# Performance work log

Measured on AMD Instinct MI355X. Metric: run time of the kernel, lower is better.

Reference implementation:

```python
import jax, jax.numpy as jnp
import numpy as np

KERNEL_MUL = 2.0
KERNEL_NUM = 5


def _gaussian_kernel(source, target, kernel_mul=KERNEL_MUL, kernel_num=KERNEL_NUM):
    # total: [(n+m), d]
    total = jnp.concatenate([source, target], axis=0)
    n_total = total.shape[0]
    # Pairwise squared L2 via GEMM trick (same math as (total0-total1)^2.sum(-1)).
    sq = jnp.sum(total * total, axis=1)  # [(n+m)]
    l2 = sq[:, None] + sq[None, :] - 2.0 * (total @ total.T)
    l2 = jnp.maximum(l2, 0.0)  # numerical floor; exact value is >= 0
    # Bandwidth from mean off-diagonal distance; .data in torch => stop_gradient.
    denom = n_total * n_total - n_total
    bandwidth = jax.lax.stop_gradient(jnp.sum(l2)) / denom
    bandwidth = bandwidth / (kernel_mul ** (kernel_num // 2))
    # Multi-bandwidth Gaussian kernel sum (fused accumulation).
    kernels = jnp.zeros_like(l2)
    for i in range(kernel_num):
        kernels = kernels + jnp.exp(-l2 / (bandwidth * (kernel_mul ** i)))
    return kernels


def setup_inputs() -> dict:
    key = jax.random.key(0)
    k1, k2 = jax.random.split(key)
    source = jax.random.normal(k1, (4096, 512), dtype=jnp.float32)
    target = jax.random.normal(k2, (4096, 512), dtype=jnp.float32)
    return {"source": source, "target": target}


def reference(source, target):
    batch_size = source.shape[0]
    kernels = _gaussian_kernel(source, target)
    xx = jnp.mean(kernels[:batch_size, :batch_size])
    yy = jnp.mean(kernels[batch_size:, batch_size:])
    xy = jnp.mean(kernels[:batch_size, batch_size:])
    yx = jnp.mean(kernels[batch_size:, :batch_size])
    return xx + yy - xy - yx
```

## Files before the change

kernel.cpp:

```cpp
#include <hip/hip_runtime.h>

#define N_TOT 8192
#define DIMS  512

typedef __attribute__((ext_vector_type(4))) int   i32x4;
typedef __attribute__((ext_vector_type(4))) float f32x4;

__global__ __launch_bounds__(256) void prep_kernel(
    const float* __restrict__ src, const float* __restrict__ tgt,
    char* __restrict__ Tb, float* __restrict__ sq,
    float* __restrict__ colsum4, float* __restrict__ sumsqtot)
{
    __shared__ float cp[4 * 512];
    __shared__ float wss[4];
    int lane = threadIdx.x & 63;
    int wave = threadIdx.x >> 6;
    int b = blockIdx.x;

    float colacc[8];
#pragma unroll
    for (int j = 0; j < 8; j++) colacc[j] = 0.f;
    float wsum = 0.f;

#pragma unroll 4
    for (int rr = 0; rr < 8; rr++) {
        int row = b * 32 + wave * 8 + rr;
        const float* p = (row < 4096) ? (src + (size_t)row * DIMS)
                                      : (tgt + (size_t)(row - 4096) * DIMS);
        float4 v0 = *(const float4*)(p + lane * 8);
        float4 v1 = *(const float4*)(p + lane * 8 + 4);
        float vs[8] = {v0.x, v0.y, v0.z, v0.w, v1.x, v1.y, v1.z, v1.w};
        float rs = 0.f;
        int q[8];
#pragma unroll
        for (int j = 0; j < 8; j++) {
            rs += vs[j] * vs[j];
            colacc[j] += vs[j];
            q[j] = max(-127, min(127, __float2int_rn(vs[j] * 25.4f)));
        }
        unsigned lo = (q[0] & 0xff) | ((q[1] & 0xff) << 8) | ((q[2] & 0xff) << 16) | ((q[3] & 0xff) << 24);
        unsigned hi = (q[4] & 0xff) | ((q[5] & 0xff) << 8) | ((q[6] & 0xff) << 16) | ((q[7] & 0xff) << 24);
        *(uint2*)(Tb + (size_t)row * DIMS + lane * 8) = make_uint2(lo, hi);
#pragma unroll
        for (int off = 32; off; off >>= 1) rs += __shfl_down(rs, off, 64);
        if (lane == 0) { sq[row] = rs; wsum += rs; }
    }
    if (lane == 0) wss[wave] = wsum;
#pragma unroll
    for (int j = 0; j < 8; j++) cp[wave * 512 + lane * 8 + j] = colacc[j];
    __syncthreads();
    int t = threadIdx.x;
    float c0 = cp[t] + cp[512 + t] + cp[1024 + t] + cp[1536 + t];
    float c1 = cp[t + 256] + cp[512 + t + 256] + cp[1024 + t + 256] + cp[1536 + t + 256];
    int rep = (b & 3) * 512;
    atomicAdd(&colsum4[rep + t], c0);
    atomicAdd(&colsum4[rep + t + 256], c1);
    if (t == 0) atomicAdd(sumsqtot, wss[0] + wss[1] + wss[2] + wss[3]);
}

__global__ __launch_bounds__(256, 4) void mmd_main(
    const char* __restrict__ Tb, const float* __restrict__ sq,
    const float* __restrict__ colsum4, const float* __restrict__ sumsqtot,
    double* __restrict__ partial)
{
    int bb = blockIdx.x;
    int x = bb & 7;
    int c = bb >> 3;
    int lo = 4 * x;
    int hi = 60 - 4 * x;
    int I, J;
    int R1 = 8 * (4 * x + 1);
    if (c < R1) {
        J = 63 - (c >> 3);
        int r = c & 7;
        I = (r < 4) ? (lo + r) : (hi + (r - 4));
    } else {
        int c2 = c - R1;
        if (c2 < 18) {
            int r;
            if (c2 < 7)       { J = hi + 2; r = c2; }
            else if (c2 < 13) { J = hi + 1; r = c2 - 7; }
            else              { J = hi;     r = c2 - 13; }
            I = (r < 4) ? (lo + r) : (hi + (r - 4));
        } else {
            int c3 = c2 - 18;
            int S3 = 4 * (57 - 8 * x);
            if (c3 < S3) {
                J = (hi - 1) - (c3 >> 2);
                I = lo + (c3 & 3);
            } else {
                int c4 = c3 - S3;
                if (c4 < 3)      { J = lo + 2; I = lo + c4; }
                else if (c4 < 5) { J = lo + 1; I = lo + (c4 - 3); }
                else             { J = lo;     I = lo; }
            }
        }
    }

    __shared__ __align__(16) char As[128 * 128];
    __shared__ __align__(16) char Bs[128 * 128];

    int t = threadIdx.x;
    int lane = t & 63, wave = t >> 6;
    int wr = (wave >> 1) * 64, wc = (wave & 1) * 64;
    int m = lane & 15, quad = lane >> 4;

    const char* Arow = Tb + (size_t)I * 128 * DIMS;
    const char* Brow = Tb + (size_t)J * 128 * DIMS;
    int lgrp = lane >> 3;
    int gsw  = ((lane & 7) ^ lgrp) * 16;

    i32x4 acc[4][4] = {};

    for (int k0 = 0; k0 < 512; k0 += 128) {
#pragma unroll
        for (int p = 0; p < 4; p++) {
            int r = p * 32 + wave * 8 + lgrp;
            const char* ga = Arow + (size_t)r * DIMS + k0 + gsw;
            const char* gb = Brow + (size_t)r * DIMS + k0 + gsw;
            __builtin_amdgcn_global_load_lds(
                (const __attribute__((address_space(1))) void*)ga,
                (__attribute__((address_space(3))) void*)&As[(p * 32 + wave * 8) * 128], 16, 0, 0);
            __builtin_amdgcn_global_load_lds(
                (const __attribute__((address_space(1))) void*)gb,
                (__attribute__((address_space(3))) void*)&Bs[(p * 32 + wave * 8) * 128], 16, 0, 0);
        }
        __syncthreads();
#pragma unroll
        for (int ks = 0; ks < 2; ks++) {
            i32x4 af[4], bfr[4];
#pragma unroll
            for (int mi = 0; mi < 4; mi++) {
                int ra = wr + mi * 16 + m;
                af[mi] = *(const i32x4*)&As[ra * 128 + ((ks * 4 + quad) ^ (m & 7)) * 16];
            }
#pragma unroll
            for (int ni = 0; ni < 4; ni++) {
                int rb = wc + ni * 16 + m;
                bfr[ni] = *(const i32x4*)&Bs[rb * 128 + ((ks * 4 + quad) ^ (m & 7)) * 16];
            }
#pragma unroll
            for (int mi = 0; mi < 4; mi++)
#pragma unroll
                for (int ni = 0; ni < 4; ni++)
                    acc[mi][ni] = __builtin_amdgcn_mfma_i32_16x16x64_i8(
                        af[mi], bfr[ni], acc[mi][ni], 0, 0, 0);
        }
        __syncthreads();
    }
    double* shd = (double*)As;
    float*  shw = (float*)(As + 64);

    float sqa[16], sqb[4];
#pragma unroll
    for (int mi = 0; mi < 4; mi++)
#pragma unroll
        for (int r = 0; r < 4; r++)
            sqa[mi * 4 + r] = sq[I * 128 + wr + mi * 16 + quad * 4 + r];
#pragma unroll
    for (int ni = 0; ni < 4; ni++) sqb[ni] = sq[J * 128 + wc + ni * 16 + m];

    {
        float cs0 = colsum4[t] + colsum4[512 + t] + colsum4[1024 + t] + colsum4[1536 + t];
        int uu = t + 256;
        float cs1 = colsum4[uu] + colsum4[512 + uu] + colsum4[1024 + uu] + colsum4[1536 + uu];
        double c2 = (double)cs0 * (double)cs0 + (double)cs1 * (double)cs1;
#pragma unroll
        for (int off = 32; off; off >>= 1) c2 += __shfl_down(c2, off, 64);
        if (lane == 0) shd[wave] = c2;
        __syncthreads();
        if (t == 0) {
            double C2 = shd[0] + shd[1] + shd[2] + shd[3];
            double SS = (double)sumsqtot[0];
            double suml2 = 2.0 * 8192.0 * SS - 2.0 * C2;
            double denom = 8192.0 * 8192.0 - 8192.0;
            shd[4] = suml2 / denom / 4.0;
        }
        __syncthreads();
    }
    double bws = shd[4];

    float nc = (float)(-1.4426950408889634 / (16.0 * bws));
    float m2nc = -2.0f * nc * (float)(25.0 / 16129.0);
    float pa[16], pb[4];
#pragma unroll
    for (int i = 0; i < 16; i++) pa[i] = nc * sqa[i];
#pragma unroll
    for (int i = 0; i < 4; i++)  pb[i] = nc * sqb[i];
    float lsum = 0.f;
    bool diag = (I == J);
    bool wdiag = diag && (wr == wc);
    int mq = m - quad * 4;
#pragma unroll
    for (int mi = 0; mi < 4; mi++) {
#pragma unroll
        for (int ni = 0; ni < 4; ni++) {
#pragma unroll
            for (int r = 0; r < 4; r++) {
                float kv;
                if (wdiag && mi == ni && r == mq) {
                    kv = 5.0f;
                } else {
                    float arg = fmaf((float)acc[mi][ni][r], m2nc, pa[mi * 4 + r] + pb[ni]);
                    float u = exp2f(arg);
                    float u2 = u * u;
                    float u4 = u2 * u2;
                    float u8 = u4 * u4;
                    float u16 = u8 * u8;
                    kv = ((u + u2) + (u4 + u8)) + u16;
                }
                lsum += kv;
            }
        }
    }
#pragma unroll
    for (int off = 32; off; off >>= 1) lsum += __shfl_down(lsum, off, 64);
    if (lane == 0) shw[wave] = lsum;
    __syncthreads();
    if (t == 0) {
        double s = (double)shw[0] + (double)shw[1] + (double)shw[2] + (double)shw[3];
        double wgt = diag ? 1.0 : 2.0;
        bool cross = (I < 32) != (J < 32);
        partial[bb] = s * wgt * (cross ? -1.0 : 1.0);
    }
}

__global__ __launch_bounds__(256) void final_kernel(
    const double* __restrict__ partial, float* __restrict__ out)
{
    int t = threadIdx.x;
    double s = 0.0;
    for (int i = t; i < 2080; i += 256) s += partial[i];
#pragma unroll
    for (int off = 32; off; off >>= 1) s += __shfl_down(s, off, 64);
    __shared__ double red[4];
    if ((t & 63) == 0) red[t >> 6] = s;
    __syncthreads();
    if (t == 0) {
        double tot = red[0] + red[1] + red[2] + red[3];
        out[0] = (float)(tot / (4096.0 * 4096.0));
    }
}

extern "C" void kernel_launch(void* const* d_in, const int* in_sizes, int n_in,
                              void* d_out, int out_size, void* d_ws, size_t ws_size,
                              hipStream_t stream) {
    const float* src = (const float*)d_in[0];
    const float* tgt = (const float*)d_in[1];
    char* ws = (char*)d_ws;
    char* Tb           = ws;
    float* sq          = (float*)(ws + 4u * 1024 * 1024);
    char* zblock       = ws + 4u * 1024 * 1024 + 32 * 1024;
    float* colsum4     = (float*)zblock;
    float* sumsqtot    = (float*)(zblock + 8192);
    double* partial    = (double*)(zblock + 8704);

    prep_kernel<<<256, 256, 0, stream>>>(src, tgt, Tb, sq, colsum4, sumsqtot);
    mmd_main<<<2080, 256, 0, stream>>>(Tb, sq, colsum4, sumsqtot, partial);
    final_kernel<<<1, 256, 0, stream>>>(partial, (float*)d_out);
}
```

Measured before the change: 109.2 us.

## Load MFMA operands directly from global memory with register double-buffering

Removes the LDS staging path and per-stage barriers from the int8 GEMM tile. Each lane now loads its MFMA fragments straight from global memory into registers, prefetching the next K-slice while the current one is multiplied. Occupancy is lowered from 4 to 3 blocks per SIMD to make room for the extra registers. In exchange, the two waves sharing a row or column fetch the same data separately through the caches, and the per-lane 16-byte global reads are strided rather than coalesced.

```diff
diff --git a/kernel.cpp b/kernel.cpp
--- a/kernel.cpp
+++ b/kernel.cpp
@@ -58,7 +58,7 @@
     if (t == 0) atomicAdd(sumsqtot, wss[0] + wss[1] + wss[2] + wss[3]);
 }
 
-__global__ __launch_bounds__(256, 4) void mmd_main(
+__global__ __launch_bounds__(256, 3) void mmd_main(
     const char* __restrict__ Tb, const float* __restrict__ sq,
     const float* __restrict__ colsum4, const float* __restrict__ sumsqtot,
     double* __restrict__ partial)
@@ -97,59 +97,63 @@
         }
     }
 
-    __shared__ __align__(16) char As[128 * 128];
-    __shared__ __align__(16) char Bs[128 * 128];
-
     int t = threadIdx.x;
     int lane = t & 63, wave = t >> 6;
     int wr = (wave >> 1) * 64, wc = (wave & 1) * 64;
     int m = lane & 15, quad = lane >> 4;
 
-    const char* Arow = Tb + (size_t)I * 128 * DIMS;
-    const char* Brow = Tb + (size_t)J * 128 * DIMS;
-    int lgrp = lane >> 3;
-    int gsw  = ((lane & 7) ^ lgrp) * 16;
+    const char* Abase = Tb + (size_t)I * 128 * DIMS;
+    const char* Bbase = Tb + (size_t)J * 128 * DIMS;
+    const char* pA[4];
+    const char* pB[4];
+#pragma unroll
+    for (int mi = 0; mi < 4; mi++)
+        pA[mi] = Abase + (size_t)((wr + mi * 16 + m) * DIMS + quad * 16);
+#pragma unroll
+    for (int ni = 0; ni < 4; ni++)
+        pB[ni] = Bbase + (size_t)((wc + ni * 16 + m) * DIMS + quad * 16);
 
     i32x4 acc[4][4] = {};
-
-    for (int k0 = 0; k0 < 512; k0 += 128) {
-#pragma unroll
-        for (int p = 0; p < 4; p++) {
-            int r = p * 32 + wave * 8 + lgrp;
-            const char* ga = Arow + (size_t)r * DIMS + k0 + gsw;
-            const char* gb = Brow + (size_t)r * DIMS + k0 + gsw;
-            __builtin_amdgcn_global_load_lds(
-                (const __attribute__((address_space(1))) void*)ga,
-                (__attribute__((address_space(3))) void*)&As[(p * 32 + wave * 8) * 128], 16, 0, 0);
-            __builtin_amdgcn_global_load_lds(
-                (const __attribute__((address_space(1))) void*)gb,
-                (__attribute__((address_space(3))) void*)&Bs[(p * 32 + wave * 8) * 128], 16, 0, 0);
-        }
-        __syncthreads();
-#pragma unroll
-        for (int ks = 0; ks < 2; ks++) {
-            i32x4 af[4], bfr[4];
-#pragma unroll
-            for (int mi = 0; mi < 4; mi++) {
-                int ra = wr + mi * 16 + m;
-                af[mi] = *(const i32x4*)&As[ra * 128 + ((ks * 4 + quad) ^ (m & 7)) * 16];
-            }
-#pragma unroll
-            for (int ni = 0; ni < 4; ni++) {
-                int rb = wc + ni * 16 + m;
-                bfr[ni] = *(const i32x4*)&Bs[rb * 128 + ((ks * 4 + quad) ^ (m & 7)) * 16];
+    i32x4 af0[4], bf0[4], af1[4], bf1[4];
+
+#pragma unroll
+    for (int mi = 0; mi < 4; mi++) af0[mi] = *(const i32x4*)(pA[mi]);
+#pragma unroll
+    for (int ni = 0; ni < 4; ni++) bf0[ni] = *(const i32x4*)(pB[ni]);
+
+#pragma unroll
+    for (int s = 0; s < 8; s++) {
+        if (s & 1) {
+            if (s < 7) {
+#pragma unroll
+                for (int mi = 0; mi < 4; mi++) af0[mi] = *(const i32x4*)(pA[mi] + (s + 1) * 64);
+#pragma unroll
+                for (int ni = 0; ni < 4; ni++) bf0[ni] = *(const i32x4*)(pB[ni] + (s + 1) * 64);
             }
 #pragma unroll
             for (int mi = 0; mi < 4; mi++)
 #pragma unroll
                 for (int ni = 0; ni < 4; ni++)
                     acc[mi][ni] = __builtin_amdgcn_mfma_i32_16x16x64_i8(
-                        af[mi], bfr[ni], acc[mi][ni], 0, 0, 0);
-        }
-        __syncthreads();
-    }
-    double* shd = (double*)As;
-    float*  shw = (float*)(As + 64);
+                        af1[mi], bf1[ni], acc[mi][ni], 0, 0, 0);
+        } else {
+            if (s < 7) {
+#pragma unroll
+                for (int mi = 0; mi < 4; mi++) af1[mi] = *(const i32x4*)(pA[mi] + (s + 1) * 64);
+#pragma unroll
+                for (int ni = 0; ni < 4; ni++) bf1[ni] = *(const i32x4*)(pB[ni] + (s + 1) * 64);
+            }
+#pragma unroll
+            for (int mi = 0; mi < 4; mi++)
+#pragma unroll
+                for (int ni = 0; ni < 4; ni++)
+                    acc[mi][ni] = __builtin_amdgcn_mfma_i32_16x16x64_i8(
+                        af0[mi], bf0[ni], acc[mi][ni], 0, 0, 0);
+        }
+    }
+
+    __shared__ double shd[9];
+    __shared__ float  shw[4];
 
     float sqa[16], sqb[4];
 #pragma unroll
@@ -174,11 +178,11 @@
             double SS = (double)sumsqtot[0];
             double suml2 = 2.0 * 8192.0 * SS - 2.0 * C2;
             double denom = 8192.0 * 8192.0 - 8192.0;
-            shd[4] = suml2 / denom / 4.0;
+            shd[8] = suml2 / denom / 4.0;
         }
         __syncthreads();
     }
-    double bws = shd[4];
+    double bws = shd[8];
 
     float nc = (float)(-1.4426950408889634 / (16.0 * bws));
     float m2nc = -2.0f * nc * (float)(25.0 / 16129.0);
```

New measurement: 146.7 us. 1.34x slower.
